# Performance work log

Measured on AMD Instinct MI355X. Metric: run time of the kernel, lower is better.

Reference implementation:

```python
import jax, jax.numpy as jnp
import numpy as np

B, T, N_EMBED, HEAD_SIZE = 8, 2048, 1024, 64
NEG_INF = float('-inf')


def setup_inputs() -> dict:
    key = jax.random.key(0)
    ks = jax.random.split(key, 6)
    k = jax.random.normal(ks[0], (B, T, N_EMBED), dtype=jnp.float32)
    q = jax.random.normal(ks[1], (B, T, N_EMBED), dtype=jnp.float32)
    v = jax.random.normal(ks[2], (B, T, N_EMBED), dtype=jnp.float32)
    mask = jnp.ones((B, T), dtype=jnp.int32)  # 1 = attendable key position
    scale = 1.0 / np.sqrt(N_EMBED)  # keep logits well-scaled
    Wk = jax.random.normal(ks[3], (HEAD_SIZE, N_EMBED), dtype=jnp.float32) * scale
    Wq = jax.random.normal(ks[4], (HEAD_SIZE, N_EMBED), dtype=jnp.float32) * scale
    Wv = jax.random.normal(ks[5], (HEAD_SIZE, N_EMBED), dtype=jnp.float32) * scale
    return {"k": k, "q": q, "v": v, "mask": mask, "Wk": Wk, "Wq": Wq, "Wv": Wv}


def reference(k, q, v, mask, Wk, Wq, Wv):
    # Linear projections (bias=False): x @ W.T, W is [head_size, n_embed]
    kh = jnp.einsum('btd,hd->bth', k, Wk)  # [B,T,H]
    qh = jnp.einsum('btd,hd->bth', q, Wq)  # [B,T,H]
    vh = jnp.einsum('btd,hd->bth', v, Wv)  # [B,T,H]

    # Scaled scores: q @ k^T * head_size**-0.5 -> [B,T,T]
    wei = jnp.einsum('bqh,bkh->bqk', qh, kh) * (HEAD_SIZE ** -0.5)

    # Causal (look-ahead) mask
    Tq = k.shape[1]
    causal = jnp.tril(jnp.ones((Tq, Tq), dtype=bool))
    wei = jnp.where(causal[None, :, :], wei, NEG_INF)

    # Custom key mask: mask [B,T] broadcast over query dim (mask.unsqueeze(1))
    wei = jnp.where(mask[:, None, :] == 0, NEG_INF, wei)

    wei = jax.nn.softmax(wei, axis=-1)
    # dropout p=0.0 -> identity
    out = jnp.einsum('bqk,bkh->bqh', wei, vh)  # [B,T,H]
    return out
```

## Files before the change

### kernel.cpp

```cpp
#include <hip/hip_runtime.h>
#include <hip/hip_bf16.h>

#define NB 8
#define NT 2048
#define NE 1024
#define NH 64

typedef __bf16 bf16_t;
typedef __bf16 bf16x8 __attribute__((ext_vector_type(8)));
typedef float f32x4 __attribute__((ext_vector_type(4)));

#define MFMA16(a, b, c) __builtin_amdgcn_mfma_f32_16x16x32_bf16(a, b, c, 0, 0, 0)

static __device__ __forceinline__ f32x4 fzero4() {
    f32x4 z = {0.f, 0.f, 0.f, 0.f};
    return z;
}

static __device__ __forceinline__ void gload_lds16(const void* gsrc, void* ldst) {
    __builtin_amdgcn_global_load_lds(
        (const __attribute__((address_space(1))) char*)gsrc,
        (__attribute__((address_space(3))) char*)ldst, 16, 0, 0);
}

__global__ __launch_bounds__(256) void convw_kernel(
    const float* __restrict__ Wq, const float* __restrict__ Wk,
    const float* __restrict__ Wv, bf16_t* __restrict__ Wb)
{
    int src = blockIdx.y;
    const float* W = (src == 0) ? Wq : ((src == 1) ? Wk : Wv);
    int idx = (blockIdx.x * 256 + threadIdx.x) * 8;
    f32x4 a = *(const f32x4*)(W + idx);
    f32x4 b = *(const f32x4*)(W + idx + 4);
    bf16x8 o;
#pragma unroll
    for (int j = 0; j < 4; ++j) { o[j] = (bf16_t)a[j]; o[4 + j] = (bf16_t)b[j]; }
    *(bf16x8*)(Wb + (size_t)src * (NH * NE) + idx) = o;
}

__global__ __launch_bounds__(256) void proj_kernel(
    const float* __restrict__ q_in, const float* __restrict__ k_in,
    const float* __restrict__ v_in, const bf16_t* __restrict__ Wb,
    bf16_t* __restrict__ qh, bf16_t* __restrict__ kh, bf16_t* __restrict__ vhT)
{
    const int which = blockIdx.y;
    const int w    = threadIdx.x >> 6;
    const int lane = threadIdx.x & 63;
    const int l15  = lane & 15;
    const int lhi  = lane >> 4;
    const int t0   = blockIdx.x * 16;

    const float*  x = (which == 0) ? q_in : ((which == 1) ? k_in : v_in);
    const bf16_t* W = Wb + (size_t)which * (NH * NE);
    const int kbeg = w * 256;

    __shared__ __align__(16) union {
        char  stage[4][2][2048];
        float mq[4][16][65];
        float mv[4][64][17];
    } sm;

    const float* xsrc0;
    const float* xsrc1;
    {
        int row = lane >> 3, phys = lane & 7;
        xsrc0 = x + (size_t)(t0 + row) * NE + kbeg + (phys ^ (row & 7)) * 4;
        int cid = 64 + lane;
        row = cid >> 3; phys = cid & 7;
        xsrc1 = x + (size_t)(t0 + row) * NE + kbeg + (phys ^ (row & 7)) * 4;
    }
    const bf16_t* wrow = W + (size_t)l15 * NE + kbeg + lhi * 8;

    const int xo0 = l15 * 128 + (((lhi * 2 + 0) ^ (l15 & 7)) * 16);
    const int xo1 = l15 * 128 + (((lhi * 2 + 1) ^ (l15 & 7)) * 16);

    f32x4 acc[4] = {fzero4(), fzero4(), fzero4(), fzero4()};

    gload_lds16(xsrc0, &sm.stage[w][0][0]);
    gload_lds16(xsrc1, &sm.stage[w][0][1024]);

#pragma unroll
    for (int step = 0; step < 8; ++step) {
        const int cur = step & 1;
        const int k0  = step * 32;

        if (step < 7) {
            gload_lds16(xsrc0 + k0 + 32, &sm.stage[w][cur ^ 1][0]);
            gload_lds16(xsrc1 + k0 + 32, &sm.stage[w][cur ^ 1][1024]);
        }
        bf16x8 wf0 = *(const bf16x8*)(wrow + (size_t)0 * 16 * NE + k0);
        bf16x8 wf1 = *(const bf16x8*)(wrow + (size_t)1 * 16 * NE + k0);
        bf16x8 wf2 = *(const bf16x8*)(wrow + (size_t)2 * 16 * NE + k0);
        bf16x8 wf3 = *(const bf16x8*)(wrow + (size_t)3 * 16 * NE + k0);

        if (step < 7) asm volatile("s_waitcnt vmcnt(6)" ::: "memory");
        else          asm volatile("s_waitcnt vmcnt(4)" ::: "memory");

        const char* xb = &sm.stage[w][cur][0];
        f32x4 a0 = *(const f32x4*)(xb + xo0);
        f32x4 a1 = *(const f32x4*)(xb + xo1);
        bf16x8 xf;
#pragma unroll
        for (int j = 0; j < 4; ++j) { xf[j] = (bf16_t)a0[j]; xf[4 + j] = (bf16_t)a1[j]; }

        if (which < 2) {
            acc[0] = MFMA16(xf, wf0, acc[0]);
            acc[1] = MFMA16(xf, wf1, acc[1]);
            acc[2] = MFMA16(xf, wf2, acc[2]);
            acc[3] = MFMA16(xf, wf3, acc[3]);
        } else {
            acc[0] = MFMA16(wf0, xf, acc[0]);
            acc[1] = MFMA16(wf1, xf, acc[1]);
            acc[2] = MFMA16(wf2, xf, acc[2]);
            acc[3] = MFMA16(wf3, xf, acc[3]);
        }
    }

    __syncthreads();

    if (which < 2) {
#pragma unroll
        for (int cg = 0; cg < 4; ++cg)
#pragma unroll
            for (int r = 0; r < 4; ++r)
                sm.mq[w][lhi * 4 + r][cg * 16 + l15] = acc[cg][r];
        __syncthreads();
        bf16_t* outp = (which == 0) ? qh : kh;
        const int col = w * 16 + l15;
#pragma unroll
        for (int r = 0; r < 4; ++r) {
            int row = lhi * 4 + r;
            float v = sm.mq[0][row][col] + sm.mq[1][row][col] +
                      sm.mq[2][row][col] + sm.mq[3][row][col];
            outp[(size_t)(t0 + row) * NH + col] = (bf16_t)v;
        }
    } else {
#pragma unroll
        for (int hg = 0; hg < 4; ++hg)
#pragma unroll
            for (int r = 0; r < 4; ++r)
                sm.mv[w][hg * 16 + lhi * 4 + r][l15] = acc[hg][r];
        __syncthreads();
        const int tg = t0 + l15;
        const int b  = tg >> 11;
        const int tt = tg & 2047;
#pragma unroll
        for (int r = 0; r < 4; ++r) {
            int h = w * 16 + lhi * 4 + r;
            float v = sm.mv[0][h][l15] + sm.mv[1][h][l15] +
                      sm.mv[2][h][l15] + sm.mv[3][h][l15];
            vhT[(((size_t)(b * NH + h)) << 11) + tt] = (bf16_t)v;
        }
    }
}

__global__ __launch_bounds__(256) void attn_kernel(
    const bf16_t* __restrict__ qh, const bf16_t* __restrict__ kh,
    const bf16_t* __restrict__ vhT, const int* __restrict__ mask,
    float* __restrict__ out)
{
    const int lin  = blockIdx.x;
    const int qt16 = lin >> 3;
    const int b    = lin & 7;
    const int w    = threadIdx.x >> 6;
    const int lane = threadIdx.x & 63;
    const int l15  = lane & 15;
    const int lhi  = lane >> 4;

    __shared__ __align__(16) char plds[4][2][2048];
    __shared__ float sm_o[4][16][65];
    __shared__ float sm_ml[4][2][16];

    const int q0  = qt16 * 16;
    const int nkt = (q0 + 15) / 64 + 1;
    const int len = (nkt + 3) >> 2;
    const int kt_beg = w * len;
    const int kt_end = min(kt_beg + len, nkt);

    const bf16_t* qbase = qh + (size_t)(b * NT + q0 + l15) * NH + lhi * 8;
    bf16x8 qf0 = *(const bf16x8*)(qbase);
    bf16x8 qf1 = *(const bf16x8*)(qbase + 32);

    f32x4 acc_o[4] = {fzero4(), fzero4(), fzero4(), fzero4()};
    float m[4]    = {-1e30f, -1e30f, -1e30f, -1e30f};
    float lsum[4] = {0.f, 0.f, 0.f, 0.f};

    const int qq0 = q0 + lhi * 4;

    for (int kt = kt_beg; kt < kt_end; ++kt) {
        const bf16_t* kbase = kh + (size_t)(b * NT + kt * 64 + l15) * NH + lhi * 8;
        f32x4 s[4] = {fzero4(), fzero4(), fzero4(), fzero4()};
#pragma unroll
        for (int cg = 0; cg < 4; ++cg) {
            bf16x8 kf0 = *(const bf16x8*)(kbase + (size_t)cg * 16 * NH);
            bf16x8 kf1 = *(const bf16x8*)(kbase + (size_t)cg * 16 * NH + 32);
            s[cg] = MFMA16(qf0, kf0, s[cg]);
            s[cg] = MFMA16(qf1, kf1, s[cg]);
        }

        int mk[4];
#pragma unroll
        for (int cg = 0; cg < 4; ++cg) mk[cg] = mask[b * NT + kt * 64 + cg * 16 + l15];
#pragma unroll
        for (int cg = 0; cg < 4; ++cg) {
            int kk = kt * 64 + cg * 16 + l15;
#pragma unroll
            for (int r = 0; r < 4; ++r) {
                float sv = s[cg][r] * 0.125f;
                bool ok = (kk <= qq0 + r) && (mk[cg] != 0);
                s[cg][r] = ok ? sv : -1e30f;
            }
        }

        float mx[4];
#pragma unroll
        for (int r = 0; r < 4; ++r) {
            mx[r] = fmaxf(fmaxf(s[0][r], s[1][r]), fmaxf(s[2][r], s[3][r]));
#pragma unroll
            for (int d = 1; d < 16; d <<= 1) mx[r] = fmaxf(mx[r], __shfl_xor(mx[r], d));
        }
        float resc[4];
#pragma unroll
        for (int r = 0; r < 4; ++r) {
            float mn = fmaxf(m[r], mx[r]);
            resc[r] = __expf(m[r] - mn);
            m[r] = mn;
        }
        float rs[4] = {0.f, 0.f, 0.f, 0.f};
#pragma unroll
        for (int cg = 0; cg < 4; ++cg)
#pragma unroll
            for (int r = 0; r < 4; ++r) {
                float sv = s[cg][r];
                float p = (sv > -5e29f) ? __expf(sv - m[r]) : 0.f;
                s[cg][r] = p;
                rs[r] += p;
            }
#pragma unroll
        for (int r = 0; r < 4; ++r) {
#pragma unroll
            for (int d = 1; d < 16; d <<= 1) rs[r] += __shfl_xor(rs[r], d);
            lsum[r] = lsum[r] * resc[r] + rs[r];
        }
#pragma unroll
        for (int cg = 0; cg < 4; ++cg)
#pragma unroll
            for (int r = 0; r < 4; ++r) acc_o[cg][r] *= resc[r];

        char* pb = &plds[w][kt & 1][0];
#pragma unroll
        for (int cg = 0; cg < 4; ++cg)
#pragma unroll
            for (int r = 0; r < 4; ++r) {
                int row = lhi * 4 + r;
                int col = cg * 16 + l15;
                int byte = (row * 128 + col * 2) ^ ((row & 7) << 4);
                *(bf16_t*)(pb + byte) = (bf16_t)s[cg][r];
            }

        const bf16_t* vbase = vhT + ((size_t)(b * NH + l15) << 11) + kt * 64 + lhi * 8;
#pragma unroll
        for (int kc = 0; kc < 2; ++kc) {
            int row = l15;
            int byte = (row * 128 + kc * 64 + lhi * 16) ^ ((row & 7) << 4);
            bf16x8 pf = *(bf16x8*)(pb + byte);
#pragma unroll
            for (int cg = 0; cg < 4; ++cg) {
                bf16x8 vf = *(const bf16x8*)(vbase + ((size_t)cg * 16 << 11) + kc * 32);
                acc_o[cg] = MFMA16(pf, vf, acc_o[cg]);
            }
        }
    }

#pragma unroll
    for (int cg = 0; cg < 4; ++cg)
#pragma unroll
        for (int r = 0; r < 4; ++r)
            sm_o[w][lhi * 4 + r][cg * 16 + l15] = acc_o[cg][r];
    if (l15 == 0) {
#pragma unroll
        for (int r = 0; r < 4; ++r) {
            sm_ml[w][0][lhi * 4 + r] = m[r];
            sm_ml[w][1][lhi * 4 + r] = lsum[r];
        }
    }
    __syncthreads();

#pragma unroll
    for (int r = 0; r < 4; ++r) {
        int row = lhi * 4 + r;
        float mg = -1e30f;
#pragma unroll
        for (int s = 0; s < 4; ++s) mg = fmaxf(mg, sm_ml[s][0][row]);
        float lg = 0.f, og = 0.f;
#pragma unroll
        for (int s = 0; s < 4; ++s) {
            float e = __expf(sm_ml[s][0][row] - mg);
            lg += e * sm_ml[s][1][row];
            og += e * sm_o[s][row][w * 16 + l15];
        }
        out[(size_t)(b * NT + q0 + row) * NH + w * 16 + l15] = og / lg;
    }
}

extern "C" void kernel_launch(void* const* d_in, const int* in_sizes, int n_in,
                              void* d_out, int out_size, void* d_ws, size_t ws_size,
                              hipStream_t stream)
{
    const float* k_in = (const float*)d_in[0];
    const float* q_in = (const float*)d_in[1];
    const float* v_in = (const float*)d_in[2];
    const int*   mask = (const int*)d_in[3];
    const float* Wk   = (const float*)d_in[4];
    const float* Wq   = (const float*)d_in[5];
    const float* Wv   = (const float*)d_in[6];
    float* out = (float*)d_out;

    char* ws = (char*)d_ws;
    bf16_t* Wb  = (bf16_t*)ws;
    bf16_t* qh  = (bf16_t*)(ws + 3 * NH * NE * 2);
    bf16_t* kh  = qh + (size_t)NB * NT * NH;
    bf16_t* vhT = kh + (size_t)NB * NT * NH;

    convw_kernel<<<dim3(32, 3), 256, 0, stream>>>(Wq, Wk, Wv, Wb);
    proj_kernel<<<dim3(NB * NT / 16, 3), 256, 0, stream>>>(q_in, k_in, v_in, Wb, qh, kh, vhT);
    attn_kernel<<<dim3(NB * NT / 16), 256, 0, stream>>>(qh, kh, vhT, mask, out);
}
```

Measured before the change: 106.0 us.

## Load full X tile into LDS up front and preload all weight fragments

Replaces the per-wave double-buffered 32-column staging loop in the projection kernel with one bulk load. All 16 rows of 1024 floats go into a shared LDS tile using row-contiguous, XOR-swizzled lanes, and every wave's weight fragments are loaded into registers before a single barrier. This puts all memory requests in flight at once and drops the per-step vmcnt waits, at the cost of a larger LDS footprint (64 KB) and 32 bf16x8 weight registers per thread. Occupancy may fall.

```diff
diff --git a/kernel.cpp b/kernel.cpp
--- a/kernel.cpp
+++ b/kernel.cpp
@@ -52,67 +52,53 @@
 
     const float*  x = (which == 0) ? q_in : ((which == 1) ? k_in : v_in);
     const bf16_t* W = Wb + (size_t)which * (NH * NE);
-    const int kbeg = w * 256;
 
     __shared__ __align__(16) union {
-        char  stage[4][2][2048];
+        char  stage[16][4096];
         float mq[4][16][65];
         float mv[4][64][17];
     } sm;
 
-    const float* xsrc0;
-    const float* xsrc1;
-    {
-        int row = lane >> 3, phys = lane & 7;
-        xsrc0 = x + (size_t)(t0 + row) * NE + kbeg + (phys ^ (row & 7)) * 4;
-        int cid = 64 + lane;
-        row = cid >> 3; phys = cid & 7;
-        xsrc1 = x + (size_t)(t0 + row) * NE + kbeg + (phys ^ (row & 7)) * 4;
-    }
-    const bf16_t* wrow = W + (size_t)l15 * NE + kbeg + lhi * 8;
-
-    const int xo0 = l15 * 128 + (((lhi * 2 + 0) ^ (l15 & 7)) * 16);
-    const int xo1 = l15 * 128 + (((lhi * 2 + 1) ^ (l15 & 7)) * 16);
+#pragma unroll
+    for (int j = 0; j < 16; ++j) {
+        const int row = w * 4 + (j >> 2);
+        const int q   = j & 3;
+        const float* src = x + (size_t)(t0 + row) * NE + q * 256
+                             + (lane ^ (row & 15)) * 4;
+        gload_lds16(src, &sm.stage[row][q * 1024]);
+    }
+
+    const bf16_t* wbase = W + (size_t)l15 * NE + w * 256 + lhi * 8;
+    bf16x8 wf[8][4];
+#pragma unroll
+    for (int s = 0; s < 8; ++s)
+#pragma unroll
+        for (int cg = 0; cg < 4; ++cg)
+            wf[s][cg] = *(const bf16x8*)(wbase + (size_t)cg * 16 * NE + s * 32);
+
+    __syncthreads();
 
     f32x4 acc[4] = {fzero4(), fzero4(), fzero4(), fzero4()};
 
-    gload_lds16(xsrc0, &sm.stage[w][0][0]);
-    gload_lds16(xsrc1, &sm.stage[w][0][1024]);
-
-#pragma unroll
-    for (int step = 0; step < 8; ++step) {
-        const int cur = step & 1;
-        const int k0  = step * 32;
-
-        if (step < 7) {
-            gload_lds16(xsrc0 + k0 + 32, &sm.stage[w][cur ^ 1][0]);
-            gload_lds16(xsrc1 + k0 + 32, &sm.stage[w][cur ^ 1][1024]);
-        }
-        bf16x8 wf0 = *(const bf16x8*)(wrow + (size_t)0 * 16 * NE + k0);
-        bf16x8 wf1 = *(const bf16x8*)(wrow + (size_t)1 * 16 * NE + k0);
-        bf16x8 wf2 = *(const bf16x8*)(wrow + (size_t)2 * 16 * NE + k0);
-        bf16x8 wf3 = *(const bf16x8*)(wrow + (size_t)3 * 16 * NE + k0);
-
-        if (step < 7) asm volatile("s_waitcnt vmcnt(6)" ::: "memory");
-        else          asm volatile("s_waitcnt vmcnt(4)" ::: "memory");
-
-        const char* xb = &sm.stage[w][cur][0];
-        f32x4 a0 = *(const f32x4*)(xb + xo0);
-        f32x4 a1 = *(const f32x4*)(xb + xo1);
+#pragma unroll
+    for (int s = 0; s < 8; ++s) {
+        const int c0 = w * 64 + s * 8 + lhi * 2;
+        f32x4 a0 = *(const f32x4*)(&sm.stage[l15][((c0    ) ^ (l15 & 15)) * 16]);
+        f32x4 a1 = *(const f32x4*)(&sm.stage[l15][((c0 + 1) ^ (l15 & 15)) * 16]);
         bf16x8 xf;
 #pragma unroll
         for (int j = 0; j < 4; ++j) { xf[j] = (bf16_t)a0[j]; xf[4 + j] = (bf16_t)a1[j]; }
 
         if (which < 2) {
-            acc[0] = MFMA16(xf, wf0, acc[0]);
-            acc[1] = MFMA16(xf, wf1, acc[1]);
-            acc[2] = MFMA16(xf, wf2, acc[2]);
-            acc[3] = MFMA16(xf, wf3, acc[3]);
+            acc[0] = MFMA16(xf, wf[s][0], acc[0]);
+            acc[1] = MFMA16(xf, wf[s][1], acc[1]);
+            acc[2] = MFMA16(xf, wf[s][2], acc[2]);
+            acc[3] = MFMA16(xf, wf[s][3], acc[3]);
         } else {
-            acc[0] = MFMA16(wf0, xf, acc[0]);
-            acc[1] = MFMA16(wf1, xf, acc[1]);
-            acc[2] = MFMA16(wf2, xf, acc[2]);
-            acc[3] = MFMA16(wf3, xf, acc[3]);
+            acc[0] = MFMA16(wf[s][0], xf, acc[0]);
+            acc[1] = MFMA16(wf[s][1], xf, acc[1]);
+            acc[2] = MFMA16(wf[s][2], xf, acc[2]);
+            acc[3] = MFMA16(wf[s][3], xf, acc[3]);
         }
     }
 
```

Result: slower. 117.1 us (+10.5%).
